# Kernel optimization log

Measured on AMD Instinct MI355X. Metric: run time of the kernel, lower is better.

The kernel has to match this reference:

```python
import jax, jax.numpy as jnp
import numpy as np

IN_FEATURES = 4096
OUT_FEATURES = 4096
INPUT_SCALE = 0.05
OUTPUT_SCALE = 0.05


def setup_inputs() -> dict:
    key = jax.random.key(0)
    k_x, k_w, k_ws = jax.random.split(key, 3)
    # int8 activations (already quantized upstream in W8A8 pipeline)
    x = jax.random.randint(k_x, (4, 2048, IN_FEATURES), -128, 128, dtype=jnp.int32).astype(jnp.int8)
    # simulate per-tensor absmax quantization of an fp32 weight
    w_fp = jax.random.normal(k_w, (OUT_FEATURES, IN_FEATURES), dtype=jnp.float32) * 0.02
    weight_scale = jnp.max(jnp.abs(w_fp)) / 127.0
    w_int8 = jnp.clip(jnp.round(w_fp / weight_scale), -128, 127).astype(jnp.int8)
    weight = w_int8.T  # stored as [in_features, out_features], matching int8_weight.t()
    a = jnp.array([[INPUT_SCALE / OUTPUT_SCALE]], dtype=jnp.float32)
    b = jnp.reshape(weight_scale.astype(jnp.float32), (1, 1))
    return {"x": x, "weight": weight, "a": a, "b": b}


def reference(x, weight, a, b):
    # round and saturate back to int8 (output dtype == x.dtype == int8).
    x_shape = x.shape
    x2 = x.reshape(-1, x_shape[-1]).astype(jnp.int32)          # [N, D]
    acc = jnp.matmul(x2, weight.astype(jnp.int32))             # [N, O] int32 accum
    scale = (a * b)[0, 0]                                      # alpha = in_scale*w_scale/out_scale
    y = jnp.clip(jnp.round(acc.astype(jnp.float32) * scale), -128.0, 127.0).astype(jnp.int8)
    return y.reshape(*x_shape[:-1], -1)
```

## Files before the change

kernel.cpp:

```cpp
#include <hip/hip_runtime.h>
#include <stdint.h>

typedef __attribute__((ext_vector_type(4))) int int4v;
typedef __attribute__((ext_vector_type(16))) int int16v;
typedef __attribute__((ext_vector_type(4))) uint32_t uint4v;

#define M_DIM 8192
#define N_DIM 4096
#define K_DIM 4096


__global__ void pack_a_perm(const int* __restrict__ x, uint4v* __restrict__ a8) {
    const int g = blockIdx.x * blockDim.x + threadIdx.x;
    const int w0 = (g & 3) * 4;
    const int chunk = g >> 2;
    const int* base = x + (size_t)chunk * 64;
    int4v L[4];
#pragma unroll
    for (int j = 0; j < 4; ++j) L[j] = *(const int4v*)(base + j * 16 + w0);
    uint4v outv;
#pragma unroll
    for (int wi = 0; wi < 4; ++wi) {
        outv[wi] = (uint32_t)(L[0][wi] & 0xff) | ((uint32_t)(L[1][wi] & 0xff) << 8) |
                   ((uint32_t)(L[2][wi] & 0xff) << 16) | ((uint32_t)(L[3][wi] & 0xff) << 24);
    }
    a8[g] = outv;
}

__global__ void transpose_b_perm(const int* __restrict__ w, int8_t* __restrict__ bt) {
    const int t = threadIdx.x;
    const int kt = blockIdx.y * 64;
    const int n0 = blockIdx.x * 64;
    const int c4 = t & 3;
    const int n = t >> 2;
    const int w0 = c4 * 4;
    const int* col = w + (size_t)kt * N_DIM + n0 + n;
    uint4v outv;
#pragma unroll
    for (int wi = 0; wi < 4; ++wi) {
        uint32_t p = 0;
#pragma unroll
        for (int j = 0; j < 4; ++j) {
            uint32_t b = (uint32_t)(col[(size_t)(w0 + wi + 16 * j) * N_DIM] & 0xff);
            p |= b << (8 * j);
        }
        outv[wi] = p;
    }
    *(uint4v*)&bt[(size_t)(n0 + n) * K_DIM + kt + w0 * 4] = outv;
}

__device__ inline void async16(const void* g, void* l) {
    __builtin_amdgcn_global_load_lds(
        (const __attribute__((address_space(1))) uint32_t*)g,
        (__attribute__((address_space(3))) uint32_t*)l, 16, 0, 0);
}

__global__ void __launch_bounds__(256, 4)
gemm_kernel(const int8_t* __restrict__ A, const int8_t* __restrict__ Bt,
            const float* __restrict__ pa, const float* __restrict__ pb,
            int* __restrict__ out) {
    __shared__ int8_t smem[32768];
    int8_t* As = smem;
    int8_t* Bs = smem + 16384;

    const int t = threadIdx.x;
    const int lane = t & 63;
    const int wave = t >> 6;
    const int m0 = blockIdx.y * 128;
    const int n0 = blockIdx.x * 128;
    const int wm = (wave >> 1) * 64;
    const int wn = (wave & 1) * 64;

    int16v acc[2][2];
#pragma unroll
    for (int i = 0; i < 2; ++i)
#pragma unroll
        for (int j = 0; j < 2; ++j)
#pragma unroll
            for (int r = 0; r < 16; ++r) acc[i][j][r] = 0;

    const int srow = lane >> 3;
    const int sslot = lane & 7;
    const uint32_t oStage = (uint32_t)(wave * 8 + srow) * K_DIM + ((sslot ^ srow) * 16);
    const uint32_t ldsStage = (uint32_t)(wave * 8) * 128;
    const int8_t* Ab = A + (size_t)m0 * K_DIM;
    const int8_t* Bb = Bt + (size_t)n0 * K_DIM;

    const int l31 = lane & 31;
    const int fg = lane >> 5;
    const int c7 = l31 & 7;
    const uint32_t aoff = (uint32_t)(wm + l31) * 128;
    const uint32_t boff = (uint32_t)(wn + l31) * 128;

    for (int kt = 0; kt < K_DIM; kt += 128) {
        __syncthreads();
#pragma unroll
        for (int s = 0; s < 4; ++s) {
            async16(Ab + oStage + kt + s * (32 * K_DIM), As + ldsStage + s * 4096);
            async16(Bb + oStage + kt + s * (32 * K_DIM), Bs + ldsStage + s * 4096);
        }
        __syncthreads();

#pragma unroll
        for (int ks = 0; ks < 4; ++ks) {
            const uint32_t cs = (uint32_t)(((ks * 2 + fg) ^ c7) * 16);
            int4v af[2], bf[2];
#pragma unroll
            for (int i = 0; i < 2; ++i) {
                af[i] = *(const int4v*)&As[aoff + i * 4096 + cs];
                bf[i] = *(const int4v*)&Bs[boff + i * 4096 + cs];
            }
#pragma unroll
            for (int i = 0; i < 2; ++i)
#pragma unroll
                for (int j = 0; j < 2; ++j)
                    acc[i][j] = __builtin_amdgcn_mfma_i32_32x32x32_i8(af[i], bf[j],
                                                                       acc[i][j], 0, 0, 0);
        }
    }

    const float scale = pa[0] * pb[0];
    const int col = lane & 31;
    const int rbase = (lane >> 5) * 4;
#pragma unroll
    for (int i = 0; i < 2; ++i)
#pragma unroll
        for (int j = 0; j < 2; ++j)
#pragma unroll
            for (int r = 0; r < 16; ++r) {
                const int rowf = rbase + (r & 3) + 8 * (r >> 2);
                float v = (float)acc[i][j][r] * scale;
                v = rintf(v);
                v = fminf(127.f, fmaxf(-128.f, v));
                out[(size_t)(m0 + wm + i * 32 + rowf) * N_DIM +
                    (n0 + wn + j * 32 + col)] = (int)v;
            }
}

extern "C" void kernel_launch(void* const* d_in, const int* in_sizes, int n_in,
                              void* d_out, int out_size, void* d_ws, size_t ws_size,
                              hipStream_t stream) {
    const int* x = (const int*)d_in[0];
    const int* w = (const int*)d_in[1];
    const float* pa = (const float*)d_in[2];
    const float* pb = (const float*)d_in[3];
    int* out = (int*)d_out;

    int8_t* a8 = (int8_t*)d_ws;
    int8_t* bt8 = a8 + (size_t)M_DIM * K_DIM;

    const int nwords_a = M_DIM * K_DIM / 16;
    pack_a_perm<<<nwords_a / 256, 256, 0, stream>>>(x, (uint4v*)a8);
    transpose_b_perm<<<dim3(N_DIM / 64, K_DIM / 64), 256, 0, stream>>>(w, bt8);
    gemm_kernel<<<dim3(N_DIM / 128, M_DIM / 128), 256, 0, stream>>>(a8, bt8, pa, pb, out);
}
```

Before: 407.1 us.

## Double-buffer LDS tiles and replace block barriers with per-wave LDS flag sync

Doubles shared memory to two stages so the next K tile's global-to-LDS loads are issued while the current tile is consumed by MFMAs. The two __syncthreads per iteration are replaced by LDS atomic counters: each wave signals when its async loads land and when it has finished reading a buffer. The aim is to hide load latency and avoid full-block stalls. In exchange, occupancy drops to 2 blocks per CU, waves spin-wait on LDS flags, and correctness depends on the waitcnt encoding and on memory ordering of the async loads.

```diff
diff --git a/kernel.cpp b/kernel.cpp
--- a/kernel.cpp
+++ b/kernel.cpp
@@ -55,13 +55,16 @@
         (__attribute__((address_space(3))) uint32_t*)l, 16, 0, 0);
 }
 
-__global__ void __launch_bounds__(256, 4)
+__device__ __forceinline__ void wait_ge(uint32_t* f, uint32_t tgt) {
+    while (__hip_atomic_load(f, __ATOMIC_ACQUIRE, __HIP_MEMORY_SCOPE_WORKGROUP) < tgt) {}
+}
+
+__global__ void __launch_bounds__(256, 2)
 gemm_kernel(const int8_t* __restrict__ A, const int8_t* __restrict__ Bt,
             const float* __restrict__ pa, const float* __restrict__ pb,
             int* __restrict__ out) {
-    __shared__ int8_t smem[32768];
-    int8_t* As = smem;
-    int8_t* Bs = smem + 16384;
+    __shared__ int8_t smem[65536 + 64];
+    uint32_t* flags = (uint32_t*)(smem + 65536);
 
     const int t = threadIdx.x;
     const int lane = t & 63;
@@ -70,6 +73,9 @@
     const int n0 = blockIdx.x * 128;
     const int wm = (wave >> 1) * 64;
     const int wn = (wave & 1) * 64;
+
+    if (t < 4) flags[t] = 0;
+    __syncthreads();
 
     int16v acc[2][2];
 #pragma unroll
@@ -92,23 +98,46 @@
     const uint32_t aoff = (uint32_t)(wm + l31) * 128;
     const uint32_t boff = (uint32_t)(wn + l31) * 128;
 
-    for (int kt = 0; kt < K_DIM; kt += 128) {
-        __syncthreads();
+    const bool sig = (lane == 0);
+
 #pragma unroll
-        for (int s = 0; s < 4; ++s) {
-            async16(Ab + oStage + kt + s * (32 * K_DIM), As + ldsStage + s * 4096);
-            async16(Bb + oStage + kt + s * (32 * K_DIM), Bs + ldsStage + s * 4096);
+    for (int s = 0; s < 4; ++s) {
+        async16(Ab + oStage + s * (32 * K_DIM), smem + ldsStage + s * 4096);
+        async16(Bb + oStage + s * (32 * K_DIM), smem + 32768 + ldsStage + s * 4096);
+    }
+    __builtin_amdgcn_s_waitcnt(0x0F70);
+    if (sig) __hip_atomic_fetch_add(&flags[0], 1u, __ATOMIC_RELEASE, __HIP_MEMORY_SCOPE_WORKGROUP);
+
+    const int NT = K_DIM / 128;
+#pragma unroll 2
+    for (int tt = 0; tt < NT; ++tt) {
+        const int p = tt & 1;
+        const int q = p ^ 1;
+
+        if (tt + 1 < NT) {
+            wait_ge(&flags[2 + q], 4u * (uint32_t)((tt + 1) >> 1));
+            const uint32_t koffs = (uint32_t)(tt + 1) * 128;
+#pragma unroll
+            for (int s = 0; s < 4; ++s) {
+                async16(Ab + oStage + koffs + s * (32 * K_DIM),
+                        smem + q * 16384 + ldsStage + s * 4096);
+                async16(Bb + oStage + koffs + s * (32 * K_DIM),
+                        smem + 32768 + q * 16384 + ldsStage + s * 4096);
+            }
         }
-        __syncthreads();
 
+        wait_ge(&flags[p], 4u * (uint32_t)((tt >> 1) + 1));
+
+        const int8_t* Asp = smem + p * 16384;
+        const int8_t* Bsp = smem + 32768 + p * 16384;
 #pragma unroll
         for (int ks = 0; ks < 4; ++ks) {
             const uint32_t cs = (uint32_t)(((ks * 2 + fg) ^ c7) * 16);
             int4v af[2], bf[2];
 #pragma unroll
             for (int i = 0; i < 2; ++i) {
-                af[i] = *(const int4v*)&As[aoff + i * 4096 + cs];
-                bf[i] = *(const int4v*)&Bs[boff + i * 4096 + cs];
+                af[i] = *(const int4v*)&Asp[aoff + i * 4096 + cs];
+                bf[i] = *(const int4v*)&Bsp[boff + i * 4096 + cs];
             }
 #pragma unroll
             for (int i = 0; i < 2; ++i)
@@ -116,6 +145,13 @@
                 for (int j = 0; j < 2; ++j)
                     acc[i][j] = __builtin_amdgcn_mfma_i32_32x32x32_i8(af[i], bf[j],
                                                                        acc[i][j], 0, 0, 0);
+        }
+
+        if (sig) __hip_atomic_fetch_add(&flags[2 + p], 1u, __ATOMIC_RELEASE, __HIP_MEMORY_SCOPE_WORKGROUP);
+
+        if (tt + 1 < NT) {
+            __builtin_amdgcn_s_waitcnt(0x0F70);
+            if (sig) __hip_atomic_fetch_add(&flags[q], 1u, __ATOMIC_RELEASE, __HIP_MEMORY_SCOPE_WORKGROUP);
         }
     }
 
```

Result: slower. 424.8 us (+4.4%).
